# Kernel tuning notes

Hardware: AMD Instinct MI355X
Metric: run time of the kernel (lower is better)

## Reference

```python
import jax, jax.numpy as jnp
import numpy as np

B, T_CACHE, N_STATE, N_HEAD = 128, 448, 1280, 20
HEAD_DIM = N_STATE // N_HEAD


def setup_inputs() -> dict:
    key = jax.random.key(0)
    ks = jax.random.split(key, 10)
    s = 1.0 / np.sqrt(N_STATE)
    return {
        "x": jax.random.normal(ks[0], (B, 1, N_STATE), jnp.float32),
        "k_cache": jax.random.normal(ks[1], (B, T_CACHE, N_STATE), jnp.float32),
        "v_cache": jax.random.normal(ks[2], (B, T_CACHE, N_STATE), jnp.float32),
        "mask": jnp.zeros((1, T_CACHE), jnp.float32),
        "Wq": jax.random.normal(ks[3], (N_STATE, N_STATE), jnp.float32) * s,
        "bq": jax.random.normal(ks[4], (N_STATE,), jnp.float32) * s,
        "Wk": jax.random.normal(ks[5], (N_STATE, N_STATE), jnp.float32) * s,
        "Wv": jax.random.normal(ks[6], (N_STATE, N_STATE), jnp.float32) * s,
        "bv": jax.random.normal(ks[7], (N_STATE,), jnp.float32) * s,
        "Wo": jax.random.normal(ks[8], (N_STATE, N_STATE), jnp.float32) * s,
        "bo": jax.random.normal(ks[9], (N_STATE,), jnp.float32) * s,
    }


def reference(x, k_cache, v_cache, mask, Wq, bq, Wk, Wv, bv, Wo, bo):
    b, q_len, n_state = x.shape  # q_len == 1 in loop (streaming) mode
    h, d = N_HEAD, n_state // N_HEAD

    # Q/K/V projections (Whisper: key has no bias)
    q = x @ Wq + bq                         # [B, 1, n_state]
    k = x @ Wk                              # [B, 1, n_state]
    v = x @ Wv + bv                         # [B, 1, n_state]

    # streaming KV-cache shift-and-append
    k_cache = jnp.concatenate([k_cache[:, 1:, :], k], axis=1)  # [B, T, n_state]
    v_cache = jnp.concatenate([v_cache[:, 1:, :], v], axis=1)

    t = k_cache.shape[1]
    scale = d ** (-0.25)
    qh = q.reshape(b, q_len, h, d).transpose(0, 2, 1, 3) * scale   # [B, H, q, d]
    kh = k_cache.reshape(b, t, h, d).transpose(0, 2, 3, 1) * scale  # [B, H, d, T]
    vh = v_cache.reshape(b, t, h, d).transpose(0, 2, 1, 3)          # [B, H, T, d]

    qk = jnp.matmul(qh, kh) + mask          # [B, H, q, T]
    qk = qk.astype(jnp.float32)
    w = jax.nn.softmax(qk, axis=-1).astype(qh.dtype)
    wv = jnp.matmul(w, vh)                  # [B, H, q, d]
    wv = wv.transpose(0, 2, 1, 3).reshape(b, q_len, n_state)

    out = wv @ Wo + bo                      # [B, q, n_state]
    return out, k_cache, v_cache
```

## Files before the change

kernel.cpp:

```cpp
#include <hip/hip_runtime.h>
#include <cstddef>

#define NSTATE 1280
#define TCACHE 448
#define NBATCH 128
#define NHEAD  20
#define HDIM   64
#define NT     8
#define RPC    (TCACHE / NT)

typedef float f4 __attribute__((ext_vector_type(4)));

__device__ __forceinline__ void gemm_body(const float* __restrict__ A,
                                          const float* __restrict__ B,
                                          const float* __restrict__ bias,
                                          float* __restrict__ C, size_t ldc,
                                          int kb, int ke, float scale)
{
    __shared__ float As[32][64];
    __shared__ float Bs[32][32];
    const int tid = threadIdx.x;
    const int m0 = blockIdx.y * 64;
    const int n0 = blockIdx.x * 32;
    const int tr = tid >> 4;
    const int tc = tid & 15;
    float acc[4][2] = {{0.f,0.f},{0.f,0.f},{0.f,0.f},{0.f,0.f}};

    for (int k0 = kb; k0 < ke; k0 += 32) {
        #pragma unroll
        for (int j = 0; j < 2; ++j) {
            int chunk = tid * 2 + j;
            int row   = chunk >> 3;
            int kc    = (chunk & 7) << 2;
            float4 a = *(const float4*)(A + (size_t)(m0 + row) * NSTATE + k0 + kc);
            As[kc+0][row] = a.x; As[kc+1][row] = a.y;
            As[kc+2][row] = a.z; As[kc+3][row] = a.w;
        }
        {
            int row = tid >> 3;
            int nc  = (tid & 7) << 2;
            float4 b4 = *(const float4*)(B + (size_t)(k0 + row) * NSTATE + n0 + nc);
            *(float4*)&Bs[row][nc] = b4;
        }
        __syncthreads();
        #pragma unroll
        for (int kk = 0; kk < 32; ++kk) {
            float4 a = *(const float4*)&As[kk][tr << 2];
            float2 b = *(const float2*)&Bs[kk][tc << 1];
            acc[0][0] = fmaf(a.x, b.x, acc[0][0]); acc[0][1] = fmaf(a.x, b.y, acc[0][1]);
            acc[1][0] = fmaf(a.y, b.x, acc[1][0]); acc[1][1] = fmaf(a.y, b.y, acc[1][1]);
            acc[2][0] = fmaf(a.z, b.x, acc[2][0]); acc[2][1] = fmaf(a.z, b.y, acc[2][1]);
            acc[3][0] = fmaf(a.w, b.x, acc[3][0]); acc[3][1] = fmaf(a.w, b.y, acc[3][1]);
        }
        __syncthreads();
    }
    const int n = n0 + (tc << 1);
    const float b0 = bias ? bias[n]   : 0.f;
    const float b1 = bias ? bias[n+1] : 0.f;
    #pragma unroll
    for (int i = 0; i < 4; ++i) {
        size_t m = (size_t)(m0 + (tr << 2) + i);
        C[m * ldc + n]     = (acc[i][0] + b0) * scale;
        C[m * ldc + n + 1] = (acc[i][1] + b1) * scale;
    }
}

__global__ void __launch_bounds__(256) proj_qkv_kernel(
    const float* __restrict__ x,
    const float* __restrict__ Wq, const float* __restrict__ bq,
    const float* __restrict__ Wk,
    const float* __restrict__ Wv, const float* __restrict__ bv,
    float* __restrict__ q_ws, float* __restrict__ kout, float* __restrict__ vout)
{
    const int z = blockIdx.z;
    if (z == 0) {
        gemm_body(x, Wq, bq, q_ws, NSTATE, 0, NSTATE, 0.125f);
    } else if (z == 1) {
        gemm_body(x, Wk, nullptr, kout + (size_t)(TCACHE-1) * NSTATE,
                  (size_t)TCACHE * NSTATE, 0, NSTATE, 1.0f);
    } else {
        gemm_body(x, Wv, bv, vout + (size_t)(TCACHE-1) * NSTATE,
                  (size_t)TCACHE * NSTATE, 0, NSTATE, 1.0f);
    }
}

__global__ void __launch_bounds__(320) fused_stream_kernel(
    const float* __restrict__ kin, const float* __restrict__ vin,
    const float* __restrict__ q_ws, const float* __restrict__ mask,
    float* __restrict__ kout, float* __restrict__ vout,
    float* __restrict__ pvp, float* __restrict__ m_ws, float* __restrict__ s_ws)
{
    const int tc = blockIdx.x, b = blockIdx.y;
    const int tid = threadIdx.x;
    const int h = tid >> 4, l = tid & 15;
    const int col = tid << 2;
    const size_t base = (size_t)b * TCACHE * NSTATE;
    const int t0 = tc * RPC;
    const int nrows = (tc == NT - 1) ? RPC - 1 : RPC;

    __shared__ float sc[NHEAD][RPC];

    const float4 q4 = *(const float4*)(q_ws + (size_t)b * NSTATE + col);
    const float* ksrc = kin + base + (size_t)(t0 + 1) * NSTATE + col;
    const float* vsrc = vin + base + (size_t)(t0 + 1) * NSTATE + col;
    float* kdst = kout + base + (size_t)t0 * NSTATE + col;
    float* vdst = vout + base + (size_t)t0 * NSTATE + col;

    {
        int r = 0;
        for (; r + 8 <= nrows; r += 8) {
            f4 kb[8];
            #pragma unroll
            for (int j = 0; j < 8; ++j)
                kb[j] = __builtin_nontemporal_load((const f4*)(ksrc + (size_t)(r + j) * NSTATE));
            #pragma unroll
            for (int j = 0; j < 8; ++j)
                __builtin_nontemporal_store(kb[j], (f4*)(kdst + (size_t)(r + j) * NSTATE));
            #pragma unroll
            for (int j = 0; j < 8; ++j) {
                float p = kb[j][0]*q4.x + kb[j][1]*q4.y + kb[j][2]*q4.z + kb[j][3]*q4.w;
                p += __shfl_xor(p, 1); p += __shfl_xor(p, 2);
                p += __shfl_xor(p, 4); p += __shfl_xor(p, 8);
                if (l == 0) sc[h][r + j] = p + mask[t0 + r + j];
            }
        }
        for (; r < nrows; ++r) {
            f4 kv = __builtin_nontemporal_load((const f4*)(ksrc + (size_t)r * NSTATE));
            __builtin_nontemporal_store(kv, (f4*)(kdst + (size_t)r * NSTATE));
            float p = kv[0]*q4.x + kv[1]*q4.y + kv[2]*q4.z + kv[3]*q4.w;
            p += __shfl_xor(p, 1); p += __shfl_xor(p, 2);
            p += __shfl_xor(p, 4); p += __shfl_xor(p, 8);
            if (l == 0) sc[h][r] = p + mask[t0 + r];
        }
        if (tc == NT - 1) {
            const f4 kv = *(const f4*)(kout + base + (size_t)(TCACHE-1) * NSTATE + col);
            float p = kv[0]*q4.x + kv[1]*q4.y + kv[2]*q4.z + kv[3]*q4.w;
            p += __shfl_xor(p, 1); p += __shfl_xor(p, 2);
            p += __shfl_xor(p, 4); p += __shfl_xor(p, 8);
            if (l == 0) sc[h][RPC - 1] = p + mask[TCACHE - 1];
        }
    }
    __syncthreads();

    {
        float v[4];
        float m = -1e30f;
        #pragma unroll
        for (int j = 0; j < 4; ++j) {
            int r = l + 16 * j;
            v[j] = (r < RPC) ? sc[h][r] : -1e30f;
            m = fmaxf(m, v[j]);
        }
        #pragma unroll
        for (int d = 1; d <= 8; d <<= 1) m = fmaxf(m, __shfl_xor(m, d));
        float s = 0.f;
        #pragma unroll
        for (int j = 0; j < 4; ++j) {
            v[j] = __expf(v[j] - m);
            s += v[j];
        }
        #pragma unroll
        for (int d = 1; d <= 8; d <<= 1) s += __shfl_xor(s, d);
        __syncthreads();
        #pragma unroll
        for (int j = 0; j < 4; ++j) {
            int r = l + 16 * j;
            if (r < RPC) sc[h][r] = v[j];
        }
        if (l == 0) {
            m_ws[((size_t)b * NT + tc) * NHEAD + h] = m;
            s_ws[((size_t)b * NT + tc) * NHEAD + h] = s;
        }
    }
    __syncthreads();

    float ax = 0.f, ay = 0.f, az = 0.f, aw = 0.f;
    {
        int r = 0;
        for (; r + 8 <= nrows; r += 8) {
            f4 vb[8];
            #pragma unroll
            for (int j = 0; j < 8; ++j)
                vb[j] = __builtin_nontemporal_load((const f4*)(vsrc + (size_t)(r + j) * NSTATE));
            #pragma unroll
            for (int j = 0; j < 8; ++j)
                __builtin_nontemporal_store(vb[j], (f4*)(vdst + (size_t)(r + j) * NSTATE));
            #pragma unroll
            for (int j = 0; j < 8; ++j) {
                const float w = sc[h][r + j];
                ax = fmaf(w, vb[j][0], ax); ay = fmaf(w, vb[j][1], ay);
                az = fmaf(w, vb[j][2], az); aw = fmaf(w, vb[j][3], aw);
            }
        }
        for (; r < nrows; ++r) {
            f4 vv = __builtin_nontemporal_load((const f4*)(vsrc + (size_t)r * NSTATE));
            __builtin_nontemporal_store(vv, (f4*)(vdst + (size_t)r * NSTATE));
            const float w = sc[h][r];
            ax = fmaf(w, vv[0], ax); ay = fmaf(w, vv[1], ay);
            az = fmaf(w, vv[2], az); aw = fmaf(w, vv[3], aw);
        }
        if (tc == NT - 1) {
            const f4 vv = *(const f4*)(vout + base + (size_t)(TCACHE-1) * NSTATE + col);
            const float w = sc[h][RPC - 1];
            ax = fmaf(w, vv[0], ax); ay = fmaf(w, vv[1], ay);
            az = fmaf(w, vv[2], az); aw = fmaf(w, vv[3], aw);
        }
    }
    *(float4*)(pvp + ((size_t)b * NT + tc) * NSTATE + col) =
        make_float4(ax, ay, az, aw);
}

__global__ void __launch_bounds__(256) combine_kernel(
    const float* __restrict__ pvp, const float* __restrict__ m_ws,
    const float* __restrict__ s_ws, float* __restrict__ wv_ws)
{
    const size_t idx = ((size_t)blockIdx.x * 256 + threadIdx.x) * 4;
    const int b = (int)(idx / NSTATE), col = (int)(idx % NSTATE);
    const int h = col >> 6;

    float m[NT], s[NT];
    float M = -1e30f;
    #pragma unroll
    for (int c = 0; c < NT; ++c) {
        m[c] = m_ws[((size_t)b * NT + c) * NHEAD + h];
        s[c] = s_ws[((size_t)b * NT + c) * NHEAD + h];
        M = fmaxf(M, m[c]);
    }
    float S = 0.f;
    float f[NT];
    #pragma unroll
    for (int c = 0; c < NT; ++c) { f[c] = __expf(m[c] - M); S += s[c] * f[c]; }
    const float inv = 1.0f / S;

    float4 acc = make_float4(0.f, 0.f, 0.f, 0.f);
    #pragma unroll
    for (int c = 0; c < NT; ++c) {
        const float w = f[c] * inv;
        float4 a = *(const float4*)(pvp + ((size_t)b * NT + c) * NSTATE + col);
        acc.x = fmaf(w, a.x, acc.x); acc.y = fmaf(w, a.y, acc.y);
        acc.z = fmaf(w, a.z, acc.z); acc.w = fmaf(w, a.w, acc.w);
    }
    *(float4*)(wv_ws + idx) = acc;
}

__global__ void __launch_bounds__(256) outproj_kernel(
    const float* __restrict__ wv, const float* __restrict__ Wo,
    float* __restrict__ po)
{
    const int sp = blockIdx.z;
    gemm_body(wv, Wo, nullptr, po + (size_t)sp * NBATCH * NSTATE,
              NSTATE, sp * 320, sp * 320 + 320, 1.0f);
}

__global__ void __launch_bounds__(256) out_reduce_kernel(
    const float* __restrict__ po, const float* __restrict__ bo,
    float* __restrict__ out)
{
    const size_t idx = ((size_t)blockIdx.x * 256 + threadIdx.x) * 4;
    const int col = (int)(idx % NSTATE);
    float4 s = *(const float4*)(bo + col);
    #pragma unroll
    for (int c = 0; c < 4; ++c) {
        float4 a = *(const float4*)(po + (size_t)c * NBATCH * NSTATE + idx);
        s.x += a.x; s.y += a.y; s.z += a.z; s.w += a.w;
    }
    *(float4*)(out + idx) = s;
}

extern "C" void kernel_launch(void* const* d_in, const int* in_sizes, int n_in,
                              void* d_out, int out_size, void* d_ws, size_t ws_size,
                              hipStream_t stream)
{
    const float* x       = (const float*)d_in[0];
    const float* k_cache = (const float*)d_in[1];
    const float* v_cache = (const float*)d_in[2];
    const float* mask    = (const float*)d_in[3];
    const float* Wq      = (const float*)d_in[4];
    const float* bq      = (const float*)d_in[5];
    const float* Wk      = (const float*)d_in[6];
    const float* Wv      = (const float*)d_in[7];
    const float* bv      = (const float*)d_in[8];
    const float* Wo      = (const float*)d_in[9];
    const float* bo      = (const float*)d_in[10];

    float* out  = (float*)d_out;
    float* kout = out + (size_t)NBATCH * NSTATE;
    float* vout = kout + (size_t)NBATCH * TCACHE * NSTATE;

    float* ws     = (float*)d_ws;
    float* q_ws   = ws;
    float* pvp_ws = q_ws  + (size_t)NBATCH * NSTATE;
    float* m_ws   = pvp_ws + (size_t)NBATCH * NT * NSTATE;
    float* s_ws   = m_ws  + (size_t)NBATCH * NT * NHEAD;
    float* wv_ws  = s_ws  + (size_t)NBATCH * NT * NHEAD;
    float* po_ws  = wv_ws + (size_t)NBATCH * NSTATE;

    proj_qkv_kernel<<<dim3(40, 2, 3), 256, 0, stream>>>(x, Wq, bq, Wk, Wv, bv,
                                                        q_ws, kout, vout);
    fused_stream_kernel<<<dim3(NT, NBATCH), 320, 0, stream>>>(
        k_cache, v_cache, q_ws, mask, kout, vout, pvp_ws, m_ws, s_ws);
    combine_kernel<<<dim3(160), 256, 0, stream>>>(pvp_ws, m_ws, s_ws, wv_ws);
    outproj_kernel<<<dim3(40, 2, 4), 256, 0, stream>>>(wv_ws, Wo, po_ws);
    out_reduce_kernel<<<dim3(160), 256, 0, stream>>>(po_ws, bo, out);
}
```

Baseline: 304.0 us.

## Use bf16 MFMA with split-K for QKV and output projections

Replaces the scalar FP32 tiled GEMM with a bf16 MFMA (16x16x32) kernel that converts fp32 tiles to bf16 in shared memory, and applies split-K to the QKV projections too, followed by a new reduction kernel that adds biases and scaling. The aim is to cut projection GEMM time by using the matrix cores. In exchange it lowers precision to bf16 and adds a kernel launch plus partial-sum traffic. The attention stream kernel, which dominates by memory traffic, is unchanged.

New measurement: 266.4 us. 1.14x faster.

```diff
diff --git a/kernel.cpp b/kernel.cpp
--- a/kernel.cpp
+++ b/kernel.cpp
@@ -8,79 +8,113 @@
 #define HDIM   64
 #define NT     8
 #define RPC    (TCACHE / NT)
+#define KSPLIT 4
+#define KRANGE (NSTATE / KSPLIT)
 
 typedef float f4 __attribute__((ext_vector_type(4)));
-
-__device__ __forceinline__ void gemm_body(const float* __restrict__ A,
-                                          const float* __restrict__ B,
-                                          const float* __restrict__ bias,
-                                          float* __restrict__ C, size_t ldc,
-                                          int kb, int ke, float scale)
-{
-    __shared__ float As[32][64];
-    __shared__ float Bs[32][32];
+typedef float f32x4 __attribute__((ext_vector_type(4)));
+typedef short bf16x8 __attribute__((ext_vector_type(8)));
+typedef unsigned short u16;
+typedef unsigned short u16x8 __attribute__((ext_vector_type(8)));
+
+__device__ __forceinline__ u16 f2bf(float f) {
+    unsigned u = __builtin_bit_cast(unsigned, f);
+    u += 0x7fff + ((u >> 16) & 1);
+    return (u16)(u >> 16);
+}
+
+__device__ __forceinline__ void mfma_partial_body(
+    const float* __restrict__ A, const float* __restrict__ W,
+    float* __restrict__ P)
+{
+    __shared__ u16 As[128][40];
+    __shared__ u16 Bs[64][40];
     const int tid = threadIdx.x;
-    const int m0 = blockIdx.y * 64;
-    const int n0 = blockIdx.x * 32;
-    const int tr = tid >> 4;
-    const int tc = tid & 15;
-    float acc[4][2] = {{0.f,0.f},{0.f,0.f},{0.f,0.f},{0.f,0.f}};
-
-    for (int k0 = kb; k0 < ke; k0 += 32) {
-        #pragma unroll
-        for (int j = 0; j < 2; ++j) {
-            int chunk = tid * 2 + j;
-            int row   = chunk >> 3;
-            int kc    = (chunk & 7) << 2;
-            float4 a = *(const float4*)(A + (size_t)(m0 + row) * NSTATE + k0 + kc);
-            As[kc+0][row] = a.x; As[kc+1][row] = a.y;
-            As[kc+2][row] = a.z; As[kc+3][row] = a.w;
-        }
+    const int n0 = blockIdx.x * 64;
+    const int kb = blockIdx.y * KRANGE;
+    const int w = tid >> 6, l = tid & 63;
+    const int la = l & 15, kg = l >> 4;
+    const int arow = tid >> 1, akh = (tid & 1) << 4;
+    const int bkr = tid >> 3, bnc = (tid & 7) << 3;
+    f32x4 acc[8] = {};
+
+    for (int ks = 0; ks < KRANGE; ks += 32) {
         {
-            int row = tid >> 3;
-            int nc  = (tid & 7) << 2;
-            float4 b4 = *(const float4*)(B + (size_t)(k0 + row) * NSTATE + n0 + nc);
-            *(float4*)&Bs[row][nc] = b4;
+            const float* src = A + (size_t)arow * NSTATE + kb + ks + akh;
+            float4 v0 = *(const float4*)(src);
+            float4 v1 = *(const float4*)(src + 4);
+            float4 v2 = *(const float4*)(src + 8);
+            float4 v3 = *(const float4*)(src + 12);
+            u16x8 w0, w1;
+            w0[0]=f2bf(v0.x); w0[1]=f2bf(v0.y); w0[2]=f2bf(v0.z); w0[3]=f2bf(v0.w);
+            w0[4]=f2bf(v1.x); w0[5]=f2bf(v1.y); w0[6]=f2bf(v1.z); w0[7]=f2bf(v1.w);
+            w1[0]=f2bf(v2.x); w1[1]=f2bf(v2.y); w1[2]=f2bf(v2.z); w1[3]=f2bf(v2.w);
+            w1[4]=f2bf(v3.x); w1[5]=f2bf(v3.y); w1[6]=f2bf(v3.z); w1[7]=f2bf(v3.w);
+            *(u16x8*)&As[arow][akh]     = w0;
+            *(u16x8*)&As[arow][akh + 8] = w1;
+        }
+        {
+            const float* src = W + (size_t)(kb + ks + bkr) * NSTATE + n0 + bnc;
+            float4 b0 = *(const float4*)(src);
+            float4 b1 = *(const float4*)(src + 4);
+            Bs[bnc + 0][bkr] = f2bf(b0.x); Bs[bnc + 1][bkr] = f2bf(b0.y);
+            Bs[bnc + 2][bkr] = f2bf(b0.z); Bs[bnc + 3][bkr] = f2bf(b0.w);
+            Bs[bnc + 4][bkr] = f2bf(b1.x); Bs[bnc + 5][bkr] = f2bf(b1.y);
+            Bs[bnc + 6][bkr] = f2bf(b1.z); Bs[bnc + 7][bkr] = f2bf(b1.w);
         }
         __syncthreads();
-        #pragma unroll
-        for (int kk = 0; kk < 32; ++kk) {
-            float4 a = *(const float4*)&As[kk][tr << 2];
-            float2 b = *(const float2*)&Bs[kk][tc << 1];
-            acc[0][0] = fmaf(a.x, b.x, acc[0][0]); acc[0][1] = fmaf(a.x, b.y, acc[0][1]);
-            acc[1][0] = fmaf(a.y, b.x, acc[1][0]); acc[1][1] = fmaf(a.y, b.y, acc[1][1]);
-            acc[2][0] = fmaf(a.z, b.x, acc[2][0]); acc[2][1] = fmaf(a.z, b.y, acc[2][1]);
-            acc[3][0] = fmaf(a.w, b.x, acc[3][0]); acc[3][1] = fmaf(a.w, b.y, acc[3][1]);
+        const bf16x8 bf = *(const bf16x8*)&Bs[w * 16 + la][kg * 8];
+        #pragma unroll
+        for (int mf = 0; mf < 8; ++mf) {
+            bf16x8 af = *(const bf16x8*)&As[mf * 16 + la][kg * 8];
+            acc[mf] = __builtin_amdgcn_mfma_f32_16x16x32_bf16(af, bf, acc[mf], 0, 0, 0);
         }
         __syncthreads();
     }
-    const int n = n0 + (tc << 1);
-    const float b0 = bias ? bias[n]   : 0.f;
-    const float b1 = bias ? bias[n+1] : 0.f;
-    #pragma unroll
-    for (int i = 0; i < 4; ++i) {
-        size_t m = (size_t)(m0 + (tr << 2) + i);
-        C[m * ldc + n]     = (acc[i][0] + b0) * scale;
-        C[m * ldc + n + 1] = (acc[i][1] + b1) * scale;
-    }
-}
-
-__global__ void __launch_bounds__(256) proj_qkv_kernel(
+    const int col = n0 + w * 16 + la;
+    #pragma unroll
+    for (int mf = 0; mf < 8; ++mf)
+        #pragma unroll
+        for (int j = 0; j < 4; ++j)
+            P[(size_t)(mf * 16 + kg * 4 + j) * NSTATE + col] = acc[mf][j];
+}
+
+__global__ void __launch_bounds__(256) proj_mfma_kernel(
     const float* __restrict__ x,
-    const float* __restrict__ Wq, const float* __restrict__ bq,
-    const float* __restrict__ Wk,
-    const float* __restrict__ Wv, const float* __restrict__ bv,
-    float* __restrict__ q_ws, float* __restrict__ kout, float* __restrict__ vout)
+    const float* __restrict__ Wq, const float* __restrict__ Wk,
+    const float* __restrict__ Wv, float* __restrict__ pp)
 {
     const int z = blockIdx.z;
-    if (z == 0) {
-        gemm_body(x, Wq, bq, q_ws, NSTATE, 0, NSTATE, 0.125f);
-    } else if (z == 1) {
-        gemm_body(x, Wk, nullptr, kout + (size_t)(TCACHE-1) * NSTATE,
-                  (size_t)TCACHE * NSTATE, 0, NSTATE, 1.0f);
+    const float* W = (z == 0) ? Wq : (z == 1) ? Wk : Wv;
+    mfma_partial_body(x, W,
+        pp + (size_t)(z * KSPLIT + blockIdx.y) * NBATCH * NSTATE);
+}
+
+__global__ void __launch_bounds__(256) proj_reduce_kernel(
+    const float* __restrict__ pp, const float* __restrict__ bq,
+    const float* __restrict__ bv, float* __restrict__ q_ws,
+    float* __restrict__ kout, float* __restrict__ vout)
+{
+    const int mat = blockIdx.y;
+    const size_t idx = ((size_t)blockIdx.x * 256 + threadIdx.x) * 4;
+    const int b = (int)(idx / NSTATE), col = (int)(idx % NSTATE);
+    float4 v = make_float4(0.f, 0.f, 0.f, 0.f);
+    #pragma unroll
+    for (int c = 0; c < KSPLIT; ++c) {
+        float4 a = *(const float4*)(pp + (size_t)(mat * KSPLIT + c) * NBATCH * NSTATE + idx);
+        v.x += a.x; v.y += a.y; v.z += a.z; v.w += a.w;
+    }
+    if (mat == 0) {
+        float4 bb = *(const float4*)(bq + col);
+        v.x = (v.x + bb.x) * 0.125f; v.y = (v.y + bb.y) * 0.125f;
+        v.z = (v.z + bb.z) * 0.125f; v.w = (v.w + bb.w) * 0.125f;
+        *(float4*)(q_ws + idx) = v;
+    } else if (mat == 1) {
+        *(float4*)(kout + ((size_t)b * TCACHE + TCACHE - 1) * NSTATE + col) = v;
     } else {
-        gemm_body(x, Wv, bv, vout + (size_t)(TCACHE-1) * NSTATE,
-                  (size_t)TCACHE * NSTATE, 0, NSTATE, 1.0f);
+        float4 bb = *(const float4*)(bv + col);
+        v.x += bb.x; v.y += bb.y; v.z += bb.z; v.w += bb.w;
+        *(float4*)(vout + ((size_t)b * TCACHE + TCACHE - 1) * NSTATE + col) = v;
     }
 }
 
@@ -243,13 +277,11 @@
     *(float4*)(wv_ws + idx) = acc;
 }
 
-__global__ void __launch_bounds__(256) outproj_kernel(
+__global__ void __launch_bounds__(256) outproj_mfma_kernel(
     const float* __restrict__ wv, const float* __restrict__ Wo,
     float* __restrict__ po)
 {
-    const int sp = blockIdx.z;
-    gemm_body(wv, Wo, nullptr, po + (size_t)sp * NBATCH * NSTATE,
-              NSTATE, sp * 320, sp * 320 + 320, 1.0f);
+    mfma_partial_body(wv, Wo, po + (size_t)blockIdx.y * NBATCH * NSTATE);
 }
 
 __global__ void __launch_bounds__(256) out_reduce_kernel(
@@ -260,7 +292,7 @@
     const int col = (int)(idx % NSTATE);
     float4 s = *(const float4*)(bo + col);
     #pragma unroll
-    for (int c = 0; c < 4; ++c) {
+    for (int c = 0; c < KSPLIT; ++c) {
         float4 a = *(const float4*)(po + (size_t)c * NBATCH * NSTATE + idx);
         s.x += a.x; s.y += a.y; s.z += a.z; s.w += a.w;
     }
@@ -293,13 +325,15 @@
     float* m_ws   = pvp_ws + (size_t)NBATCH * NT * NSTATE;
     float* s_ws   = m_ws  + (size_t)NBATCH * NT * NHEAD;
     float* wv_ws  = s_ws  + (size_t)NBATCH * NT * NHEAD;
-    float* po_ws  = wv_ws + (size_t)NBATCH * NSTATE;
-
-    proj_qkv_kernel<<<dim3(40, 2, 3), 256, 0, stream>>>(x, Wq, bq, Wk, Wv, bv,
-                                                        q_ws, kout, vout);
+    float* pp_ws  = wv_ws + (size_t)NBATCH * NSTATE;
+    float* po_ws  = pp_ws + (size_t)3 * KSPLIT * NBATCH * NSTATE;
+
+    proj_mfma_kernel<<<dim3(20, KSPLIT, 3), 256, 0, stream>>>(x, Wq, Wk, Wv, pp_ws);
+    proj_reduce_kernel<<<dim3(160, 3), 256, 0, stream>>>(pp_ws, bq, bv,
+                                                         q_ws, kout, vout);
     fused_stream_kernel<<<dim3(NT, NBATCH), 320, 0, stream>>>(
         k_cache, v_cache, q_ws, mask, kout, vout, pvp_ws, m_ws, s_ws);
     combine_kernel<<<dim3(160), 256, 0, stream>>>(pvp_ws, m_ws, s_ws, wv_ws);
-    outproj_kernel<<<dim3(40, 2, 4), 256, 0, stream>>>(wv_ws, Wo, po_ws);
+    outproj_mfma_kernel<<<dim3(20, KSPLIT), 256, 0, stream>>>(wv_ws, Wo, po_ws);
     out_reduce_kernel<<<dim3(160), 256, 0, stream>>>(po_ws, bo, out);
 }
```
